# Kernel tuning notes

Measured on AMD Instinct MI355X. Metric: run time of the kernel, lower is better.

## Reference

```python
import jax, jax.numpy as jnp
import numpy as np

B, N, C, O, R = 8, 1024, 768, 768, 16  # batch, tokens, in_features, out_features, rank


def setup_inputs() -> dict:
    key = jax.random.key(0)
    k1, k2, k3, k4 = jax.random.split(key, 4)
    x = jax.random.normal(k1, (B, N, C), dtype=jnp.float32)
    coef = jax.random.normal(k2, (N, R), dtype=jnp.float32)
    # params: weight (out_features, in_features, rank), bias (out_features, rank)
    weight = 0.02 * jax.random.normal(k3, (O, C, R), dtype=jnp.float32)
    bias = 0.02 * jax.random.normal(k4, (O, R), dtype=jnp.float32)
    return {"x": x, "coef": coef, "weight": weight, "bias": bias}


def reference(x, coef, weight, bias):
    # Original math: per-token weight W_n[o,c] = sum_r coef[n,r] * weight[o,c,r]
    #                out[b,n,o] = sum_c x[b,n,c] * W_n[o,c] + sum_r coef[n,r]*bias[o,r]
    # Fused form: contract in_features first, rank last; avoids the (N,O,C) tensor.
    t = jnp.einsum('bnc,ocr->bnor', x, weight)   # (B,N,O,R)
    out = jnp.einsum('bnor,nr->bno', t, coef)    # (B,N,O)
    out = out + coef @ bias.T                    # (N,O) broadcast over batch
    return out
```

## Files before the change

kernel.cpp:

```cpp
#include <hip/hip_runtime.h>

#define NN 1024
#define CC 768
#define OO 768
#define RR 16
#define MM 8192
#define KK (CC*RR)
#define BM 128
#define BO 128
#define BK 64
#define KTILES (KK/BK)
#define KSPLIT 2
#define KHALF (KTILES/KSPLIT)

typedef __bf16 bf16x8 __attribute__((ext_vector_type(8)));
typedef float  f32x4  __attribute__((ext_vector_type(4)));

__device__ static __forceinline__ void gl_lds16(const void* g, void* l) {
    __builtin_amdgcn_global_load_lds(
        (const __attribute__((address_space(1))) void*)g,
        (__attribute__((address_space(3))) void*)l,
        16, 0, 0);
}

__global__ __launch_bounds__(256) void k_prep(const float* __restrict__ w,
                                              const float* __restrict__ coef,
                                              const float* __restrict__ bias,
                                              __bf16* __restrict__ wbf,
                                              float* __restrict__ bterm,
                                              float* __restrict__ outz) {
    long id = blockIdx.x;
    if (id < 4608) {
        long u = (id * 256 + threadIdx.x) * 8;
        float4 a = *(const float4*)(w + u);
        float4 b = *(const float4*)(w + u + 4);
        bf16x8 v = {(__bf16)a.x, (__bf16)a.y, (__bf16)a.z, (__bf16)a.w,
                    (__bf16)b.x, (__bf16)b.y, (__bf16)b.z, (__bf16)b.w};
        *(bf16x8*)(wbf + u) = v;
    } else if (id < 7680) {
        int i = (int)(id - 4608) * 256 + threadIdx.x;
        int n = i / OO, o = i - n * OO;
        const float4* cp = (const float4*)(coef + n * RR);
        const float4* bp = (const float4*)(bias + o * RR);
        float s = 0.f;
#pragma unroll
        for (int q = 0; q < 4; ++q) {
            float4 c4 = cp[q], b4 = bp[q];
            s += c4.x * b4.x + c4.y * b4.y + c4.z * b4.z + c4.w * b4.w;
        }
        bterm[i] = s;
    } else {
        long u = ((id - 7680) * 256 + threadIdx.x) * 8;
        float4 z = {0.f, 0.f, 0.f, 0.f};
        *(float4*)(outz + u) = z;
        *(float4*)(outz + u + 4) = z;
    }
}

__global__ __launch_bounds__(256, 3) void k_gemm(const float* __restrict__ x,
                                                 const float* __restrict__ coef,
                                                 const __bf16* __restrict__ wbf,
                                                 const float* __restrict__ bterm,
                                                 float* __restrict__ out) {
    __shared__ __bf16 lA[BM * BK];
    __shared__ __bf16 lB[BO * BK];

    const int tid = threadIdx.x;

    int id    = blockIdx.x;
    int xcd   = id & 7;
    int slot  = id >> 3;
    int kh    = slot & 1;
    int slot2 = slot >> 1;
    int otile = slot2 >> 3;
    int mtile = xcd * 8 + (slot2 & 7);
    const int m0 = mtile * BM, o0 = otile * BO;
    const int kt0 = kh * KHALF, kt1 = kt0 + KHALF;

    const int am     = tid & 127;
    const int ahalf  = tid >> 7;
    const int m_glob = m0 + am;
    const int n_idx  = m_glob & (NN - 1);
    const float* xrow = x + (long)m_glob * CC;

    float cf[16];
#pragma unroll
    for (int r = 0; r < 16; r += 4) {
        float4 t4 = *(const float4*)(coef + n_idx * RR + r);
        cf[r] = t4.x; cf[r + 1] = t4.y; cf[r + 2] = t4.z; cf[r + 3] = t4.w;
    }

    const int lane = tid & 63, wave = tid >> 6;
    const int wm = (wave & 1) * 64, wo = (wave >> 1) * 64;
    const int lrow = lane & 15, quad = lane >> 4;

    f32x4 acc[4][4] = {};

    float2 x2 = *(const float2*)(xrow + kt0 * 4 + 2 * ahalf);

#pragma unroll 1
    for (int kt = kt0; kt < kt1; ++kt) {
#pragma unroll
        for (int s = 0; s < 4; ++s) {
            int u = s * 256 + tid;
            int row = u >> 3, cl = u & 7;
            int g = cl ^ (row & 7);
            const __bf16* gp = wbf + (long)(o0 + row) * KK + kt * BK + g * 8;
            gl_lds16(gp, ((char*)lB) + u * 16);
        }
        float2 x2n = x2;
        if (kt + 1 < kt1) x2n = *(const float2*)(xrow + (kt + 1) * 4 + 2 * ahalf);
#pragma unroll
        for (int ci = 0; ci < 2; ++ci) {
            float xv = (ci == 0) ? x2.x : x2.y;
            int c_local = 2 * ahalf + ci;
#pragma unroll
            for (int rh = 0; rh < 2; ++rh) {
                bf16x8 v;
#pragma unroll
                for (int j = 0; j < 8; ++j) v[j] = (__bf16)(xv * cf[rh * 8 + j]);
                int kb  = c_local * 2 + rh;
                int kbs = kb ^ (am & 7);
                *(bf16x8*)(&lA[am * BK + kbs * 8]) = v;
            }
        }
        x2 = x2n;
        __syncthreads();

#pragma unroll
        for (int ks = 0; ks < 2; ++ks) {
            bf16x8 af[4], bfr[4];
            int kb = ks * 4 + quad;
#pragma unroll
            for (int im = 0; im < 4; ++im) {
                int row = wm + im * 16 + lrow;
                af[im] = *(const bf16x8*)(&lA[row * BK + (kb ^ (row & 7)) * 8]);
            }
#pragma unroll
            for (int io = 0; io < 4; ++io) {
                int row = wo + io * 16 + lrow;
                bfr[io] = *(const bf16x8*)(&lB[row * BK + (kb ^ (row & 7)) * 8]);
            }
#pragma unroll
            for (int im = 0; im < 4; ++im)
#pragma unroll
                for (int io = 0; io < 4; ++io)
                    acc[im][io] = __builtin_amdgcn_mfma_f32_16x16x32_bf16(
                        af[im], bfr[io], acc[im][io], 0, 0, 0);
        }
        __syncthreads();
    }

#pragma unroll
    for (int im = 0; im < 4; ++im) {
#pragma unroll
        for (int io = 0; io < 4; ++io) {
            int o = o0 + wo + io * 16 + lrow;
#pragma unroll
            for (int r = 0; r < 4; ++r) {
                int moff = wm + im * 16 + quad * 4 + r;
                long m = m0 + moff;
                int n = (int)(m & (NN - 1));
                float v = acc[im][io][r];
                if (kh == 0) v += bterm[(long)n * OO + o];
                atomicAdd(&out[m * OO + o], v);
            }
        }
    }
}

__global__ void k_naive(const float* __restrict__ x, const float* __restrict__ coef,
                        const float* __restrict__ w, const float* __restrict__ bias,
                        float* __restrict__ out) {
    long i = (long)blockIdx.x * 256 + threadIdx.x;
    if (i >= (long)MM * OO) return;
    int o = (int)(i % OO);
    long m = i / OO;
    int n = (int)(m & (NN - 1));
    float cf[16];
#pragma unroll
    for (int r = 0; r < 16; ++r) cf[r] = coef[n * RR + r];
    const float* xr = x + m * CC;
    const float* wr = w + (long)o * CC * RR;
    float s = 0.f;
    for (int c = 0; c < CC; ++c) {
        float t = 0.f;
#pragma unroll
        for (int r = 0; r < 16; ++r) t += cf[r] * wr[c * RR + r];
        s += xr[c] * t;
    }
    float bs = 0.f;
#pragma unroll
    for (int r = 0; r < 16; ++r) bs += cf[r] * bias[o * RR + r];
    out[i] = s + bs;
}

extern "C" void kernel_launch(void* const* d_in, const int* in_sizes, int n_in,
                              void* d_out, int out_size, void* d_ws, size_t ws_size,
                              hipStream_t stream) {
    const float* x    = (const float*)d_in[0];
    const float* coef = (const float*)d_in[1];
    const float* w    = (const float*)d_in[2];
    const float* bias = (const float*)d_in[3];
    float* out = (float*)d_out;

    const size_t wbf_bytes = (size_t)OO * KK * sizeof(__bf16);
    const size_t bt_bytes  = (size_t)NN * OO * sizeof(float);

    if (ws_size >= wbf_bytes + bt_bytes) {
        __bf16* wbf  = (__bf16*)d_ws;
        float*  btrm = (float*)((char*)d_ws + wbf_bytes);
        k_prep<<<10752, 256, 0, stream>>>(w, coef, bias, wbf, btrm, out);
        k_gemm<<<768, 256, 0, stream>>>(x, coef, wbf, btrm, out);
    } else {
        k_naive<<<(int)(((long)MM * OO + 255) / 256), 256, 0, stream>>>(x, coef, w, bias, out);
    }
}
```

Before: 285.2 us.

## Pre-pack weights into MFMA fragment layout and load B directly to registers

The prep kernel now writes the bf16 weight in the exact per-lane MFMA B-fragment order, so the GEMM loads B fragments straight from global memory into registers instead of staging them through LDS. The A tile gets a double-buffered LDS array, which lets the trailing barrier be dropped. The block-to-tile mapping is also reordered so that blocks on each XCD group by output tile. This is meant to cut LDS traffic, LDS capacity and one barrier per k-step. In exchange, global load latency for B is exposed within the same iteration with no prefetch, and the two waves that share an output slice now fetch the same B data redundantly.

```diff
diff --git a/kernel.cpp b/kernel.cpp
--- a/kernel.cpp
+++ b/kernel.cpp
@@ -10,33 +10,34 @@
 #define BO 128
 #define BK 64
 #define KTILES (KK/BK)
-#define KSPLIT 2
-#define KHALF (KTILES/KSPLIT)
+#define KHALF (KTILES/2)
 
 typedef __bf16 bf16x8 __attribute__((ext_vector_type(8)));
 typedef float  f32x4  __attribute__((ext_vector_type(4)));
-
-__device__ static __forceinline__ void gl_lds16(const void* g, void* l) {
-    __builtin_amdgcn_global_load_lds(
-        (const __attribute__((address_space(1))) void*)g,
-        (__attribute__((address_space(3))) void*)l,
-        16, 0, 0);
-}
 
 __global__ __launch_bounds__(256) void k_prep(const float* __restrict__ w,
                                               const float* __restrict__ coef,
                                               const float* __restrict__ bias,
-                                              __bf16* __restrict__ wbf,
+                                              __bf16* __restrict__ bfrag,
                                               float* __restrict__ bterm,
                                               float* __restrict__ outz) {
     long id = blockIdx.x;
     if (id < 4608) {
-        long u = (id * 256 + threadIdx.x) * 8;
-        float4 a = *(const float4*)(w + u);
-        float4 b = *(const float4*)(w + u + 4);
+        long t = id * 256 + threadIdx.x;
+        int lrow = (int)(t & 15);
+        int quad = (int)((t >> 4) & 3);
+        int ks   = (int)((t >> 6) & 1);
+        int o16  = (int)((t >> 7) & 7);
+        int rest = (int)(t >> 10);
+        int kt = rest % 192, ot = rest / 192;
+        int o = ot * 128 + o16 * 16 + lrow;
+        int c = kt * 4 + ks * 2 + (quad >> 1);
+        const float* src = w + ((long)o * CC + c) * RR + (quad & 1) * 8;
+        float4 a = *(const float4*)src;
+        float4 b = *(const float4*)(src + 4);
         bf16x8 v = {(__bf16)a.x, (__bf16)a.y, (__bf16)a.z, (__bf16)a.w,
                     (__bf16)b.x, (__bf16)b.y, (__bf16)b.z, (__bf16)b.w};
-        *(bf16x8*)(wbf + u) = v;
+        *(bf16x8*)(bfrag + t * 8) = v;
     } else if (id < 7680) {
         int i = (int)(id - 4608) * 256 + threadIdx.x;
         int n = i / OO, o = i - n * OO;
@@ -59,22 +60,19 @@
 
 __global__ __launch_bounds__(256, 3) void k_gemm(const float* __restrict__ x,
                                                  const float* __restrict__ coef,
-                                                 const __bf16* __restrict__ wbf,
+                                                 const __bf16* __restrict__ bfrag,
                                                  const float* __restrict__ bterm,
                                                  float* __restrict__ out) {
-    __shared__ __bf16 lA[BM * BK];
-    __shared__ __bf16 lB[BO * BK];
+    __shared__ __bf16 lA[2][BM * BK];
 
     const int tid = threadIdx.x;
 
-    int id    = blockIdx.x;
-    int xcd   = id & 7;
-    int slot  = id >> 3;
-    int kh    = slot & 1;
-    int slot2 = slot >> 1;
-    int otile = slot2 >> 3;
-    int mtile = xcd * 8 + (slot2 & 7);
-    const int m0 = mtile * BM, o0 = otile * BO;
+    int g     = (blockIdx.x & 7) * 96 + (blockIdx.x >> 3);
+    int ot    = g >> 7;
+    int rem   = g & 127;
+    int kh    = rem & 1;
+    int mtile = rem >> 1;
+    const int m0 = mtile * BM;
     const int kt0 = kh * KHALF, kt1 = kt0 + KHALF;
 
     const int am     = tid & 127;
@@ -94,34 +92,37 @@
     const int wm = (wave & 1) * 64, wo = (wave >> 1) * 64;
     const int lrow = lane & 15, quad = lane >> 4;
 
+    const __bf16* Bk = bfrag + ((long)ot * 192 + kt0) * 8192
+                     + (wo >> 4) * 1024 + quad * 128 + lrow * 8;
+
     f32x4 acc[4][4] = {};
-
     float2 x2 = *(const float2*)(xrow + kt0 * 4 + 2 * ahalf);
 
 #pragma unroll 1
     for (int kt = kt0; kt < kt1; ++kt) {
-#pragma unroll
-        for (int s = 0; s < 4; ++s) {
-            int u = s * 256 + tid;
-            int row = u >> 3, cl = u & 7;
-            int g = cl ^ (row & 7);
-            const __bf16* gp = wbf + (long)(o0 + row) * KK + kt * BK + g * 8;
-            gl_lds16(gp, ((char*)lB) + u * 16);
-        }
+        bf16x8 bfr[2][4];
+#pragma unroll
+        for (int ks = 0; ks < 2; ++ks)
+#pragma unroll
+            for (int io = 0; io < 4; ++io)
+                bfr[ks][io] = *(const bf16x8*)(Bk + io * 1024 + ks * 512);
+        Bk += 8192;
+
         float2 x2n = x2;
         if (kt + 1 < kt1) x2n = *(const float2*)(xrow + (kt + 1) * 4 + 2 * ahalf);
+
+        __bf16* la = &lA[kt & 1][0];
 #pragma unroll
         for (int ci = 0; ci < 2; ++ci) {
-            float xv = (ci == 0) ? x2.x : x2.y;
+            float xv = ci ? x2.y : x2.x;
             int c_local = 2 * ahalf + ci;
 #pragma unroll
             for (int rh = 0; rh < 2; ++rh) {
                 bf16x8 v;
 #pragma unroll
                 for (int j = 0; j < 8; ++j) v[j] = (__bf16)(xv * cf[rh * 8 + j]);
-                int kb  = c_local * 2 + rh;
-                int kbs = kb ^ (am & 7);
-                *(bf16x8*)(&lA[am * BK + kbs * 8]) = v;
+                int kb = c_local * 2 + rh;
+                *(bf16x8*)(&la[am * BK + ((kb ^ (am & 7)) * 8)]) = v;
             }
         }
         x2 = x2n;
@@ -129,33 +130,27 @@
 
 #pragma unroll
         for (int ks = 0; ks < 2; ++ks) {
-            bf16x8 af[4], bfr[4];
+            bf16x8 af[4];
             int kb = ks * 4 + quad;
 #pragma unroll
             for (int im = 0; im < 4; ++im) {
                 int row = wm + im * 16 + lrow;
-                af[im] = *(const bf16x8*)(&lA[row * BK + (kb ^ (row & 7)) * 8]);
-            }
-#pragma unroll
-            for (int io = 0; io < 4; ++io) {
-                int row = wo + io * 16 + lrow;
-                bfr[io] = *(const bf16x8*)(&lB[row * BK + (kb ^ (row & 7)) * 8]);
+                af[im] = *(const bf16x8*)(&la[row * BK + ((kb ^ (row & 7)) * 8)]);
             }
 #pragma unroll
             for (int im = 0; im < 4; ++im)
 #pragma unroll
                 for (int io = 0; io < 4; ++io)
                     acc[im][io] = __builtin_amdgcn_mfma_f32_16x16x32_bf16(
-                        af[im], bfr[io], acc[im][io], 0, 0, 0);
-        }
-        __syncthreads();
+                        af[im], bfr[ks][io], acc[im][io], 0, 0, 0);
+        }
     }
 
 #pragma unroll
     for (int im = 0; im < 4; ++im) {
 #pragma unroll
         for (int io = 0; io < 4; ++io) {
-            int o = o0 + wo + io * 16 + lrow;
+            int o = ot * BO + wo + io * 16 + lrow;
 #pragma unroll
             for (int r = 0; r < 4; ++r) {
                 int moff = wm + im * 16 + quad * 4 + r;
@@ -204,14 +199,14 @@
     const float* bias = (const float*)d_in[3];
     float* out = (float*)d_out;
 
-    const size_t wbf_bytes = (size_t)OO * KK * sizeof(__bf16);
-    const size_t bt_bytes  = (size_t)NN * OO * sizeof(float);
-
-    if (ws_size >= wbf_bytes + bt_bytes) {
-        __bf16* wbf  = (__bf16*)d_ws;
-        float*  btrm = (float*)((char*)d_ws + wbf_bytes);
-        k_prep<<<10752, 256, 0, stream>>>(w, coef, bias, wbf, btrm, out);
-        k_gemm<<<768, 256, 0, stream>>>(x, coef, wbf, btrm, out);
+    const size_t bfrag_bytes = (size_t)OO * KK * sizeof(__bf16);
+    const size_t bt_bytes    = (size_t)NN * OO * sizeof(float);
+
+    if (ws_size >= bfrag_bytes + bt_bytes) {
+        __bf16* bfrag = (__bf16*)d_ws;
+        float*  btrm  = (float*)((char*)d_ws + bfrag_bytes);
+        k_prep<<<10752, 256, 0, stream>>>(w, coef, bias, bfrag, btrm, out);
+        k_gemm<<<768, 256, 0, stream>>>(x, coef, bfrag, btrm, out);
     } else {
         k_naive<<<(int)(((long)MM * OO + 255) / 256), 256, 0, stream>>>(x, coef, w, bias, out);
     }
```

Result: no change. 285.3 us (+0.0%).
